# Kernel optimization log

Measured on AMD Instinct MI355X. Metric: run time of the kernel, lower is better.

The kernel has to match this reference:

```python
import jax, jax.numpy as jnp
import numpy as np

DIM = 768
NUM_HEADS = 12
HEAD_DIM = DIM // NUM_HEADS
SCALE = HEAD_DIM ** -0.5


def setup_inputs() -> dict:
    key = jax.random.key(0)
    ks = jax.random.split(key, 5)
    b, n = 8, 1024
    x = jax.random.normal(ks[0], (b, n, DIM), dtype=jnp.float32)
    # qkv Linear weight: torch stores (out, in) = (3*DIM, DIM)
    w_qkv = jax.random.normal(ks[1], (3 * DIM, DIM), dtype=jnp.float32) * (DIM ** -0.5)
    q_bias = jax.random.normal(ks[2], (DIM,), dtype=jnp.float32) * 0.02
    v_bias = jax.random.normal(ks[3], (DIM,), dtype=jnp.float32) * 0.02
    w_proj = jax.random.normal(ks[4], (DIM, DIM), dtype=jnp.float32) * (DIM ** -0.5)
    b_proj = jnp.zeros((DIM,), dtype=jnp.float32)
    return {"x": x, "w_qkv": w_qkv, "q_bias": q_bias, "v_bias": v_bias,
            "w_proj": w_proj, "b_proj": b_proj}


def reference(x, w_qkv, q_bias, v_bias, w_proj, b_proj):
    b, n, _ = x.shape
    # qkv bias: [q_bias, zeros, v_bias]
    qkv_bias = jnp.concatenate([q_bias, jnp.zeros_like(v_bias), v_bias])
    qkv = x @ w_qkv.T + qkv_bias                      # (b, n, 3*DIM)
    qkv = qkv.reshape(b, n, 3, NUM_HEADS, HEAD_DIM)
    qkv = jnp.transpose(qkv, (2, 0, 3, 1, 4))          # (3, b, h, n, d)
    q, k, v = qkv[0], qkv[1], qkv[2]
    q = q * SCALE
    attn = jnp.einsum('bhqd,bhkd->bhqk', q, k)         # (b, h, n, n)
    attn = jax.nn.softmax(attn, axis=-1)
    out = jnp.einsum('bhqk,bhkd->bhqd', attn, v)       # (b, h, n, d)
    out = jnp.transpose(out, (0, 2, 1, 3)).reshape(b, n, NUM_HEADS * HEAD_DIM)
    return out @ w_proj.T + b_proj
```

## Files before the change

kernel.cpp:

```cpp
#include <hip/hip_runtime.h>
#include <math.h>

#define BATCH 8
#define SEQ   1024
#define DIM   768
#define NH    12
#define HD    64
#define MROWS 8192
#define NQKV  2304
#define KDIM  768
#define QSCALE 0.18033688011112042f

typedef unsigned short u16;
typedef unsigned int   u32;
typedef __attribute__((ext_vector_type(8))) short bf16x8;
typedef __attribute__((ext_vector_type(4))) float f32x4;
typedef __attribute__((ext_vector_type(16))) float f32x16;

__device__ __forceinline__ u16 f2bf(float f){
  u32 u = __builtin_bit_cast(u32, f);
  u += 0x7FFFu + ((u >> 16) & 1u);
  return (u16)(u >> 16);
}

__device__ __forceinline__ void gload16(const void* g, void* l){
  __builtin_amdgcn_global_load_lds((const __attribute__((address_space(1))) u32*)g,
                                   (__attribute__((address_space(3))) u32*)l, 16, 0, 0);
}

__device__ __forceinline__ f32x16 zero16(){
  return (f32x16){0.f,0.f,0.f,0.f,0.f,0.f,0.f,0.f,0.f,0.f,0.f,0.f,0.f,0.f,0.f,0.f};
}

__global__ __launch_bounds__(256) void convert_bf16(
    const float* __restrict__ x, const float* __restrict__ wq,
    const float* __restrict__ wp, u16* __restrict__ xb,
    u16* __restrict__ wqb, u16* __restrict__ wpb){
  const long n1 = (long)MROWS*DIM/8, n2 = (long)NQKV*DIM/8, n3 = (long)DIM*DIM/8;
  long i = (long)blockIdx.x*blockDim.x + threadIdx.x;
  const float* s; u16* d;
  if (i < n1)            { s = x  + i*8;        d = xb  + i*8; }
  else if (i < n1+n2)    { long j=i-n1;    s = wq + j*8; d = wqb + j*8; }
  else if (i < n1+n2+n3) { long j=i-n1-n2; s = wp + j*8; d = wpb + j*8; }
  else return;
  float4 a = ((const float4*)s)[0];
  float4 b = ((const float4*)s)[1];
  union { u16 h[8]; uint4 v; } o;
  o.h[0]=f2bf(a.x); o.h[1]=f2bf(a.y); o.h[2]=f2bf(a.z); o.h[3]=f2bf(a.w);
  o.h[4]=f2bf(b.x); o.h[5]=f2bf(b.y); o.h[6]=f2bf(b.z); o.h[7]=f2bf(b.w);
  *((uint4*)d) = o.v;
}

__global__ __launch_bounds__(256) void qkv_gemm(
    const u16* __restrict__ xb, const u16* __restrict__ wb,
    const float* __restrict__ qbias, const float* __restrict__ vbias,
    u16* __restrict__ qo, u16* __restrict__ ko, u16* __restrict__ vto){
  __shared__ u16 As[16384];
  __shared__ u16 Bs[16384];
  const int tid = threadIdx.x;
  const int wid = tid >> 6, lane = tid & 63;
  const int lr = lane & 15, lg = lane >> 4;
  const int wm = wid >> 1, wn = wid & 1;
  const int swz = (blockIdx.x & 7) * 144 + (blockIdx.x >> 3);
  const int bm = swz / 18, bn = swz % 18;
  const int mbase = bm * 128, nbase = bn * 128;
  const int sr8 = tid >> 3;
  const int sc8 = ((tid & 7) ^ (sr8 & 7)) * 8;
  const u16* aS = xb + (size_t)(mbase + sr8) * KDIM + sc8;
  const u16* bS = wb + (size_t)(nbase + sr8) * KDIM + sc8;
  u16* aD = As + tid * 8;
  u16* bD = Bs + tid * 8;

#define STAGEQ(buf, k0) do {                                                  \
    _Pragma("unroll")                                                         \
    for (int i = 0; i < 4; ++i){                                              \
      gload16(aS + (k0) + (size_t)i*32*KDIM, aD + (buf)*8192 + i*2048);       \
      gload16(bS + (k0) + (size_t)i*32*KDIM, bD + (buf)*8192 + i*2048);       \
    }                                                                         \
  } while(0)

  f32x4 acc[4][4];
  #pragma unroll
  for (int a=0;a<4;++a)
    #pragma unroll
    for (int b=0;b<4;++b) acc[a][b] = (f32x4){0.f,0.f,0.f,0.f};

  STAGEQ(0, 0);
  __syncthreads();

  for (int kt = 0; kt < 12; ++kt){
    const int cur = kt & 1;
    if (kt < 11) STAGEQ(cur ^ 1, (kt+1)*64);
    const u16* Ac = As + cur*8192;
    const u16* Bc = Bs + cur*8192;
    bf16x8 af[2][4], bfv[2][4];
    #pragma unroll
    for (int kk = 0; kk < 2; ++kk){
      #pragma unroll
      for (int f = 0; f < 4; ++f){
        const int ch = (((kk*4 + lg) ^ (lr & 7)) * 8);
        af[kk][f]  = *(const bf16x8*)(Ac + (wm*64 + f*16 + lr)*64 + ch);
        bfv[kk][f] = *(const bf16x8*)(Bc + (wn*64 + f*16 + lr)*64 + ch);
      }
    }
    #pragma unroll
    for (int fm = 0; fm < 4; ++fm)
      #pragma unroll
      for (int fn = 0; fn < 4; ++fn){
        acc[fm][fn] = __builtin_amdgcn_mfma_f32_16x16x32_bf16(af[0][fm], bfv[0][fn], acc[fm][fn], 0,0,0);
        acc[fm][fn] = __builtin_amdgcn_mfma_f32_16x16x32_bf16(af[1][fm], bfv[1][fn], acc[fm][fn], 0,0,0);
      }
    __syncthreads();
  }
#undef STAGEQ

  const int which = bn / 6;
  const int bb = mbase >> 10, nn0 = mbase & 1023;
  if (which == 2){
    const int vcol0 = nbase - 1536;
    float bv[4];
    #pragma unroll
    for (int fn = 0; fn < 4; ++fn) bv[fn] = vbias[vcol0 + wn*64 + fn*16 + lr];
    u16* Ls = As;
    #pragma unroll
    for (int h = 0; h < 2; ++h){
      __syncthreads();
      if (wm == h){
        #pragma unroll
        for (int fn = 0; fn < 4; ++fn){
          const int n = wn*64 + fn*16 + lr;
          #pragma unroll
          for (int fm = 0; fm < 4; ++fm)
            #pragma unroll
            for (int r = 0; r < 4; ++r){
              const int mloc = fm*16 + lg*4 + r;
              Ls[n*64 + (((mloc>>3) ^ (n&7))*8) + (mloc&7)] = f2bf(acc[fm][fn][r] + bv[fn]);
            }
        }
      }
      __syncthreads();
      const int n = tid >> 1, half = tid & 1;
      const int col = vcol0 + n;
      u16* drow = vto + ((size_t)((bb*NH + (col>>6))*HD + (col&63)))*SEQ + nn0 + h*64 + half*32;
      #pragma unroll
      for (int j = 0; j < 4; ++j)
        *(uint4*)(drow + j*8) = *(const uint4*)(Ls + n*64 + ((((half<<2)+j) ^ (n&7))*8));
    }
  } else {
    const int mrow0 = mbase + wm*64;
    const int ncol0 = nbase - which*768 + wn*64;
    #pragma unroll
    for (int fn = 0; fn < 4; ++fn){
      const int col = ncol0 + fn*16 + lr;
      const int hh = col >> 6, dd = col & 63;
      const float bias = (which == 0) ? qbias[col] : 0.f;
      #pragma unroll
      for (int fm = 0; fm < 4; ++fm){
        #pragma unroll
        for (int r = 0; r < 4; ++r){
          const int m = mrow0 + fm*16 + lg*4 + r;
          const int head = (m >> 10)*NH + hh;
          const float v = acc[fm][fn][r] + bias;
          if (which == 0) qo[((size_t)head*SEQ + (m & 1023))*HD + dd] = f2bf(v * QSCALE);
          else            ko[((size_t)head*SEQ + (m & 1023))*HD + dd] = f2bf(v);
        }
      }
    }
  }
}

__global__ __launch_bounds__(256, 3) void attn_kernel(
    const u16* __restrict__ qg, const u16* __restrict__ kg,
    const u16* __restrict__ vtg, u16* __restrict__ og){
  __shared__ u16 Ks[3*4096];
  __shared__ u16 VTs[3*4096];
  const int tid  = threadIdx.x;
  const int wid  = tid >> 6, lane = tid & 63;
  const int l31  = lane & 31, hi = lane >> 5, l7 = lane & 7;
  const int bid  = blockIdx.x;
  const int swz  = (bid & 7) * 96 + (bid >> 3);
  const int head = swz >> 3;
  const int qbase = (swz & 7) * 128;
  const u16* Q  = qg  + (size_t)head * SEQ * HD;
  const u16* K  = kg  + (size_t)head * SEQ * HD;
  const u16* VT = vtg + (size_t)head * HD * SEQ;

  const int qrow = qbase + wid*32 + l31;
  bf16x8 qf[4];
  #pragma unroll
  for (int dc = 0; dc < 4; ++dc)
    qf[dc] = *(const bf16x8*)(Q + (size_t)qrow*HD + dc*16 + hi*8);

  f32x16 oacc[2];
  oacc[0] = zero16(); oacc[1] = zero16();
  float lrow = 0.f;

  const int srow   = lane >> 3;
  const int schunk = ((lane & 7) ^ srow) * 8;

#define STAGE(bufi, kv0) do {                                                 \
    const u16* ksrc = K + (size_t)((kv0) + wid*16 + srow)*HD + schunk;        \
    gload16(ksrc,         &Ks[(bufi)*4096 + wid*1024]);                       \
    gload16(ksrc + 8*HD,  &Ks[(bufi)*4096 + wid*1024 + 512]);                 \
    const u16* vsrc = VT + (size_t)(wid*16 + srow)*SEQ + (kv0) + schunk;      \
    gload16(vsrc,         &VTs[(bufi)*4096 + wid*1024]);                      \
    gload16(vsrc + 8*SEQ, &VTs[(bufi)*4096 + wid*1024 + 512]);                \
  } while(0)

  STAGE(0, 0);
  STAGE(1, 64);

  #pragma unroll
  for (int t = 0; t < 16; ++t){
    const int cur = t % 3;
    if (t < 15) asm volatile("s_waitcnt vmcnt(4)" ::: "memory");
    else        asm volatile("s_waitcnt vmcnt(0)" ::: "memory");
    __builtin_amdgcn_s_barrier();
    if (t < 14) STAGE((t+2)%3, (t+2)*64);

    const u16* Kc  = &Ks[cur*4096];
    const u16* VTc = &VTs[cur*4096];

    f32x16 sv[2];
    __builtin_amdgcn_s_setprio(1);
    #pragma unroll
    for (int b = 0; b < 2; ++b){
      sv[b] = zero16();
      #pragma unroll
      for (int dc = 0; dc < 4; ++dc){
        bf16x8 kf = *(const bf16x8*)(&Kc[(b*32 + l31)*64 + (((dc*2 + hi) ^ l7) * 8)]);
        sv[b] = __builtin_amdgcn_mfma_f32_32x32x16_bf16(kf, qf[dc], sv[b], 0,0,0);
      }
    }
    __builtin_amdgcn_s_setprio(0);

    float tsum[16];
    #pragma unroll
    for (int i = 0; i < 16; ++i){
      float p0 = __builtin_amdgcn_exp2f(sv[0][i]);
      float p1 = __builtin_amdgcn_exp2f(sv[1][i]);
      sv[0][i] = p0; sv[1][i] = p1;
      tsum[i] = p0 + p1;
    }
    #pragma unroll
    for (int st = 8; st > 0; st >>= 1)
      #pragma unroll
      for (int i = 0; i < st; ++i) tsum[i] += tsum[i + st];
    const float ssum = tsum[0];
    lrow += ssum + __shfl_xor(ssum, 32);

    bf16x8 pa[4];
    #pragma unroll
    for (int b = 0; b < 2; ++b){
      u32 x0,x1,x2,x3,y0,y1,y2,y3;
      asm("v_cvt_pk_bf16_f32 %0, %1, %2" : "=v"(x0) : "v"(sv[b][0]),  "v"(sv[b][1]));
      asm("v_cvt_pk_bf16_f32 %0, %1, %2" : "=v"(y0) : "v"(sv[b][4]),  "v"(sv[b][5]));
      asm("v_cvt_pk_bf16_f32 %0, %1, %2" : "=v"(x1) : "v"(sv[b][2]),  "v"(sv[b][3]));
      asm("v_cvt_pk_bf16_f32 %0, %1, %2" : "=v"(y1) : "v"(sv[b][6]),  "v"(sv[b][7]));
      asm("v_permlane32_swap_b32 %0, %1" : "+v"(x0), "+v"(y0));
      asm("v_permlane32_swap_b32 %0, %1" : "+v"(x1), "+v"(y1));
      asm("v_cvt_pk_bf16_f32 %0, %1, %2" : "=v"(x2) : "v"(sv[b][8]),  "v"(sv[b][9]));
      asm("v_cvt_pk_bf16_f32 %0, %1, %2" : "=v"(y2) : "v"(sv[b][12]), "v"(sv[b][13]));
      asm("v_cvt_pk_bf16_f32 %0, %1, %2" : "=v"(x3) : "v"(sv[b][10]), "v"(sv[b][11]));
      asm("v_cvt_pk_bf16_f32 %0, %1, %2" : "=v"(y3) : "v"(sv[b][14]), "v"(sv[b][15]));
      asm("v_permlane32_swap_b32 %0, %1" : "+v"(x2), "+v"(y2));
      asm("v_permlane32_swap_b32 %0, %1" : "+v"(x3), "+v"(y3));
      union { u32 w[4]; bf16x8 f; } fa, fb;
      fa.w[0]=x0; fa.w[1]=x1; fa.w[2]=y0; fa.w[3]=y1;
      fb.w[0]=x2; fb.w[1]=x3; fb.w[2]=y2; fb.w[3]=y3;
      pa[b*2]   = fa.f;
      pa[b*2+1] = fb.f;
    }

    __builtin_amdgcn_s_setprio(1);
    #pragma unroll
    for (int kc = 0; kc < 4; ++kc){
      #pragma unroll
      for (int db = 0; db < 2; ++db){
        bf16x8 vf = *(const bf16x8*)(&VTc[(db*32 + l31)*64 + (((kc*2 + hi) ^ l7) * 8)]);
        oacc[db] = __builtin_amdgcn_mfma_f32_32x32x16_bf16(pa[kc], vf, oacc[db], 0,0,0);
      }
    }
    __builtin_amdgcn_s_setprio(0);
  }
#undef STAGE

  const float inv = 1.f / lrow;
  const int bb = head / NH, hh = head % NH;
  #pragma unroll
  for (int r = 0; r < 16; ++r){
    const int q = (r&3) + 8*(r>>2) + 4*hi;
    const float s = __shfl(inv, q);
    const int n = qbase + wid*32 + q;
    u16* orow = og + (size_t)(bb*SEQ + n)*DIM + hh*HD;
    orow[l31]      = f2bf(oacc[0][r] * s);
    orow[32 + l31] = f2bf(oacc[1][r] * s);
  }
}

__global__ __launch_bounds__(256) void proj_gemm(
    const u16* __restrict__ ab, const u16* __restrict__ wb,
    const float* __restrict__ bias, float* __restrict__ out){
  __shared__ u16 As[16384];
  __shared__ u16 Bs[16384];
  const int tid = threadIdx.x;
  const int wid = tid >> 6, lane = tid & 63;
  const int lr = lane & 15, lg = lane >> 4;
  const int wm = wid >> 1, wn = wid & 1;
  const int swz = (blockIdx.x & 7) * 48 + (blockIdx.x >> 3);
  const int bm = swz / 6, bn = swz % 6;
  const int mbase = bm * 128, nbase = bn * 128;
  const int sr8 = tid >> 3;
  const int sc8 = ((tid & 7) ^ (sr8 & 7)) * 8;
  const u16* aS = ab + (size_t)(mbase + sr8) * KDIM + sc8;
  const u16* bS = wb + (size_t)(nbase + sr8) * KDIM + sc8;
  u16* aD = As + tid * 8;
  u16* bD = Bs + tid * 8;

#define STAGEP(buf, k0) do {                                                  \
    _Pragma("unroll")                                                         \
    for (int i = 0; i < 4; ++i){                                              \
      gload16(aS + (k0) + (size_t)i*32*KDIM, aD + (buf)*8192 + i*2048);       \
      gload16(bS + (k0) + (size_t)i*32*KDIM, bD + (buf)*8192 + i*2048);       \
    }                                                                         \
  } while(0)

  f32x4 acc[4][4];
  #pragma unroll
  for (int a=0;a<4;++a)
    #pragma unroll
    for (int b=0;b<4;++b) acc[a][b] = (f32x4){0.f,0.f,0.f,0.f};

  STAGEP(0, 0);
  __syncthreads();

  for (int kt = 0; kt < 12; ++kt){
    const int cur = kt & 1;
    if (kt < 11) STAGEP(cur ^ 1, (kt+1)*64);
    const u16* Ac = As + cur*8192;
    const u16* Bc = Bs + cur*8192;
    bf16x8 af[2][4], bfv[2][4];
    #pragma unroll
    for (int kk = 0; kk < 2; ++kk){
      #pragma unroll
      for (int f = 0; f < 4; ++f){
        const int ch = (((kk*4 + lg) ^ (lr & 7)) * 8);
        af[kk][f]  = *(const bf16x8*)(Ac + (wm*64 + f*16 + lr)*64 + ch);
        bfv[kk][f] = *(const bf16x8*)(Bc + (wn*64 + f*16 + lr)*64 + ch);
      }
    }
    #pragma unroll
    for (int fm = 0; fm < 4; ++fm)
      #pragma unroll
      for (int fn = 0; fn < 4; ++fn){
        acc[fm][fn] = __builtin_amdgcn_mfma_f32_16x16x32_bf16(af[0][fm], bfv[0][fn], acc[fm][fn], 0,0,0);
        acc[fm][fn] = __builtin_amdgcn_mfma_f32_16x16x32_bf16(af[1][fm], bfv[1][fn], acc[fm][fn], 0,0,0);
      }
    __syncthreads();
  }
#undef STAGEP

  const int mrow0 = mbase + wm*64;
  const int ncol0 = nbase + wn*64;
  #pragma unroll
  for (int fn = 0; fn < 4; ++fn){
    const int col = ncol0 + fn*16 + lr;
    const float bv = bias[col];
    #pragma unroll
    for (int fm = 0; fm < 4; ++fm){
      #pragma unroll
      for (int r = 0; r < 4; ++r){
        const int m = mrow0 + fm*16 + lg*4 + r;
        out[(size_t)m*DIM + col] = acc[fm][fn][r] + bv;
      }
    }
  }
}

extern "C" void kernel_launch(void* const* d_in, const int* in_sizes, int n_in,
                              void* d_out, int out_size, void* d_ws, size_t ws_size,
                              hipStream_t stream) {
  const float* x      = (const float*)d_in[0];
  const float* w_qkv  = (const float*)d_in[1];
  const float* q_bias = (const float*)d_in[2];
  const float* v_bias = (const float*)d_in[3];
  const float* w_proj = (const float*)d_in[4];
  const float* b_proj = (const float*)d_in[5];
  float* out = (float*)d_out;
  char* ws = (char*)d_ws;
  u16* xb  = (u16*)(ws);
  u16* wqb = (u16*)(ws + 12582912);
  u16* wpb = (u16*)(ws + 16121856);
  u16* qbf = (u16*)(ws + 17301504);
  u16* kbf = (u16*)(ws + 29884416);
  u16* vtb = (u16*)(ws + 42467328);
  u16* abf = (u16*)(ws + 55050240);

  convert_bf16<<<4224, 256, 0, stream>>>(x, w_qkv, w_proj, xb, wqb, wpb);
  qkv_gemm   <<<64*18, 256, 0, stream>>>(xb, wqb, q_bias, v_bias, qbf, kbf, vtb);
  attn_kernel<<<96*8,  256, 0, stream>>>(qbf, kbf, vtb, abf);
  proj_gemm  <<<64*6,  256, 0, stream>>>(abf, wpb, b_proj, out);
}
```

Measured before the change: 106.7 us.

## Use 8 waves per block in QKV and projection GEMMs

Both GEMM kernels move from 256 to 512 threads per block, using a 2x4 wave grid in which each wave computes a 64x32 sub-tile instead of 64x64. Global-to-LDS staging is split across twice as many threads, and the V-transpose epilogue is remapped for four threads per row. The aim is more waves per CU to hide memory and LDS latency, at the cost of more A-fragment LDS reads per MFMA and heavier barrier synchronisation.

```diff
diff --git a/kernel.cpp b/kernel.cpp
--- a/kernel.cpp
+++ b/kernel.cpp
@@ -51,7 +51,8 @@
   *((uint4*)d) = o.v;
 }
 
-__global__ __launch_bounds__(256) void qkv_gemm(
+
+__global__ __launch_bounds__(512, 4) void qkv_gemm(
     const u16* __restrict__ xb, const u16* __restrict__ wb,
     const float* __restrict__ qbias, const float* __restrict__ vbias,
     u16* __restrict__ qo, u16* __restrict__ ko, u16* __restrict__ vto){
@@ -60,7 +61,7 @@
   const int tid = threadIdx.x;
   const int wid = tid >> 6, lane = tid & 63;
   const int lr = lane & 15, lg = lane >> 4;
-  const int wm = wid >> 1, wn = wid & 1;
+  const int wm = wid >> 2, wn = wid & 3;
   const int swz = (blockIdx.x & 7) * 144 + (blockIdx.x >> 3);
   const int bm = swz / 18, bn = swz % 18;
   const int mbase = bm * 128, nbase = bn * 128;
@@ -72,18 +73,17 @@
   u16* bD = Bs + tid * 8;
 
 #define STAGEQ(buf, k0) do {                                                  \
-    _Pragma("unroll")                                                         \
-    for (int i = 0; i < 4; ++i){                                              \
-      gload16(aS + (k0) + (size_t)i*32*KDIM, aD + (buf)*8192 + i*2048);       \
-      gload16(bS + (k0) + (size_t)i*32*KDIM, bD + (buf)*8192 + i*2048);       \
-    }                                                                         \
+    gload16(aS + (k0),            aD + (buf)*8192);                           \
+    gload16(aS + (k0) + 64*KDIM,  aD + (buf)*8192 + 4096);                    \
+    gload16(bS + (k0),            bD + (buf)*8192);                           \
+    gload16(bS + (k0) + 64*KDIM,  bD + (buf)*8192 + 4096);                    \
   } while(0)
 
-  f32x4 acc[4][4];
+  f32x4 acc[4][2];
   #pragma unroll
   for (int a=0;a<4;++a)
     #pragma unroll
-    for (int b=0;b<4;++b) acc[a][b] = (f32x4){0.f,0.f,0.f,0.f};
+    for (int b=0;b<2;++b) acc[a][b] = (f32x4){0.f,0.f,0.f,0.f};
 
   STAGEQ(0, 0);
   __syncthreads();
@@ -93,20 +93,21 @@
     if (kt < 11) STAGEQ(cur ^ 1, (kt+1)*64);
     const u16* Ac = As + cur*8192;
     const u16* Bc = Bs + cur*8192;
-    bf16x8 af[2][4], bfv[2][4];
+    bf16x8 af[2][4], bfv[2][2];
     #pragma unroll
     for (int kk = 0; kk < 2; ++kk){
-      #pragma unroll
-      for (int f = 0; f < 4; ++f){
-        const int ch = (((kk*4 + lg) ^ (lr & 7)) * 8);
+      const int ch = (((kk*4 + lg)) ^ (lr & 7)) * 8;
+      #pragma unroll
+      for (int f = 0; f < 4; ++f)
         af[kk][f]  = *(const bf16x8*)(Ac + (wm*64 + f*16 + lr)*64 + ch);
-        bfv[kk][f] = *(const bf16x8*)(Bc + (wn*64 + f*16 + lr)*64 + ch);
-      }
+      #pragma unroll
+      for (int g = 0; g < 2; ++g)
+        bfv[kk][g] = *(const bf16x8*)(Bc + (wn*32 + g*16 + lr)*64 + ch);
     }
     #pragma unroll
     for (int fm = 0; fm < 4; ++fm)
       #pragma unroll
-      for (int fn = 0; fn < 4; ++fn){
+      for (int fn = 0; fn < 2; ++fn){
         acc[fm][fn] = __builtin_amdgcn_mfma_f32_16x16x32_bf16(af[0][fm], bfv[0][fn], acc[fm][fn], 0,0,0);
         acc[fm][fn] = __builtin_amdgcn_mfma_f32_16x16x32_bf16(af[1][fm], bfv[1][fn], acc[fm][fn], 0,0,0);
       }
@@ -118,17 +119,17 @@
   const int bb = mbase >> 10, nn0 = mbase & 1023;
   if (which == 2){
     const int vcol0 = nbase - 1536;
-    float bv[4];
-    #pragma unroll
-    for (int fn = 0; fn < 4; ++fn) bv[fn] = vbias[vcol0 + wn*64 + fn*16 + lr];
+    float bv[2];
+    #pragma unroll
+    for (int fn = 0; fn < 2; ++fn) bv[fn] = vbias[vcol0 + wn*32 + fn*16 + lr];
     u16* Ls = As;
     #pragma unroll
     for (int h = 0; h < 2; ++h){
       __syncthreads();
       if (wm == h){
         #pragma unroll
-        for (int fn = 0; fn < 4; ++fn){
-          const int n = wn*64 + fn*16 + lr;
+        for (int fn = 0; fn < 2; ++fn){
+          const int n = wn*32 + fn*16 + lr;
           #pragma unroll
           for (int fm = 0; fm < 4; ++fm)
             #pragma unroll
@@ -139,18 +140,20 @@
         }
       }
       __syncthreads();
-      const int n = tid >> 1, half = tid & 1;
+      const int n = tid >> 2, q4 = tid & 3;
       const int col = vcol0 + n;
-      u16* drow = vto + ((size_t)((bb*NH + (col>>6))*HD + (col&63)))*SEQ + nn0 + h*64 + half*32;
-      #pragma unroll
-      for (int j = 0; j < 4; ++j)
-        *(uint4*)(drow + j*8) = *(const uint4*)(Ls + n*64 + ((((half<<2)+j) ^ (n&7))*8));
+      u16* drow = vto + ((size_t)((bb*NH + (col>>6))*HD + (col&63)))*SEQ + nn0 + h*64;
+      #pragma unroll
+      for (int j2 = 0; j2 < 2; ++j2){
+        const int j = q4*2 + j2;
+        *(uint4*)(drow + j*8) = *(const uint4*)(Ls + n*64 + ((j ^ (n&7))*8));
+      }
     }
   } else {
     const int mrow0 = mbase + wm*64;
-    const int ncol0 = nbase - which*768 + wn*64;
-    #pragma unroll
-    for (int fn = 0; fn < 4; ++fn){
+    const int ncol0 = nbase - which*768 + wn*32;
+    #pragma unroll
+    for (int fn = 0; fn < 2; ++fn){
       const int col = ncol0 + fn*16 + lr;
       const int hh = col >> 6, dd = col & 63;
       const float bias = (which == 0) ? qbias[col] : 0.f;
@@ -298,7 +301,7 @@
   }
 }
 
-__global__ __launch_bounds__(256) void proj_gemm(
+__global__ __launch_bounds__(512, 4) void proj_gemm(
     const u16* __restrict__ ab, const u16* __restrict__ wb,
     const float* __restrict__ bias, float* __restrict__ out){
   __shared__ u16 As[16384];
@@ -306,7 +309,7 @@
   const int tid = threadIdx.x;
   const int wid = tid >> 6, lane = tid & 63;
   const int lr = lane & 15, lg = lane >> 4;
-  const int wm = wid >> 1, wn = wid & 1;
+  const int wm = wid >> 2, wn = wid & 3;
   const int swz = (blockIdx.x & 7) * 48 + (blockIdx.x >> 3);
   const int bm = swz / 6, bn = swz % 6;
   const int mbase = bm * 128, nbase = bn * 128;
@@ -318,18 +321,17 @@
   u16* bD = Bs + tid * 8;
 
 #define STAGEP(buf, k0) do {                                                  \
-    _Pragma("unroll")                                                         \
-    for (int i = 0; i < 4; ++i){                                              \
-      gload16(aS + (k0) + (size_t)i*32*KDIM, aD + (buf)*8192 + i*2048);       \
-      gload16(bS + (k0) + (size_t)i*32*KDIM, bD + (buf)*8192 + i*2048);       \
-    }                                                                         \
+    gload16(aS + (k0),            aD + (buf)*8192);                           \
+    gload16(aS + (k0) + 64*KDIM,  aD + (buf)*8192 + 4096);                    \
+    gload16(bS + (k0),            bD + (buf)*8192);                           \
+    gload16(bS + (k0) + 64*KDIM,  bD + (buf)*8192 + 4096);                    \
   } while(0)
 
-  f32x4 acc[4][4];
+  f32x4 acc[4][2];
   #pragma unroll
   for (int a=0;a<4;++a)
     #pragma unroll
-    for (int b=0;b<4;++b) acc[a][b] = (f32x4){0.f,0.f,0.f,0.f};
+    for (int b=0;b<2;++b) acc[a][b] = (f32x4){0.f,0.f,0.f,0.f};
 
   STAGEP(0, 0);
   __syncthreads();
@@ -339,20 +341,21 @@
     if (kt < 11) STAGEP(cur ^ 1, (kt+1)*64);
     const u16* Ac = As + cur*8192;
     const u16* Bc = Bs + cur*8192;
-    bf16x8 af[2][4], bfv[2][4];
+    bf16x8 af[2][4], bfv[2][2];
     #pragma unroll
     for (int kk = 0; kk < 2; ++kk){
-      #pragma unroll
-      for (int f = 0; f < 4; ++f){
-        const int ch = (((kk*4 + lg) ^ (lr & 7)) * 8);
+      const int ch = (((kk*4 + lg)) ^ (lr & 7)) * 8;
+      #pragma unroll
+      for (int f = 0; f < 4; ++f)
         af[kk][f]  = *(const bf16x8*)(Ac + (wm*64 + f*16 + lr)*64 + ch);
-        bfv[kk][f] = *(const bf16x8*)(Bc + (wn*64 + f*16 + lr)*64 + ch);
-      }
+      #pragma unroll
+      for (int g = 0; g < 2; ++g)
+        bfv[kk][g] = *(const bf16x8*)(Bc + (wn*32 + g*16 + lr)*64 + ch);
     }
     #pragma unroll
     for (int fm = 0; fm < 4; ++fm)
       #pragma unroll
-      for (int fn = 0; fn < 4; ++fn){
+      for (int fn = 0; fn < 2; ++fn){
         acc[fm][fn] = __builtin_amdgcn_mfma_f32_16x16x32_bf16(af[0][fm], bfv[0][fn], acc[fm][fn], 0,0,0);
         acc[fm][fn] = __builtin_amdgcn_mfma_f32_16x16x32_bf16(af[1][fm], bfv[1][fn], acc[fm][fn], 0,0,0);
       }
@@ -361,9 +364,9 @@
 #undef STAGEP
 
   const int mrow0 = mbase + wm*64;
-  const int ncol0 = nbase + wn*64;
-  #pragma unroll
-  for (int fn = 0; fn < 4; ++fn){
+  const int ncol0 = nbase + wn*32;
+  #pragma unroll
+  for (int fn = 0; fn < 2; ++fn){
     const int col = ncol0 + fn*16 + lr;
     const float bv = bias[col];
     #pragma unroll
@@ -397,7 +400,7 @@
   u16* abf = (u16*)(ws + 55050240);
 
   convert_bf16<<<4224, 256, 0, stream>>>(x, w_qkv, w_proj, xb, wqb, wpb);
-  qkv_gemm   <<<64*18, 256, 0, stream>>>(xb, wqb, q_bias, v_bias, qbf, kbf, vtb);
+  qkv_gemm   <<<64*18, 512, 0, stream>>>(xb, wqb, q_bias, v_bias, qbf, kbf, vtb);
   attn_kernel<<<96*8,  256, 0, stream>>>(qbf, kbf, vtb, abf);
-  proj_gemm  <<<64*6,  256, 0, stream>>>(abf, wpb, b_proj, out);
-}
+  proj_gemm  <<<64*6,  512, 0, stream>>>(abf, wpb, b_proj, out);
+}
```

Result: no change. 105.0 us (-1.6%).
